# Kernel tuning notes

Hardware: AMD Instinct MI355X
Metric: run time of the kernel (lower is better)

Reference implementation:

```python
import jax, jax.numpy as jnp
import numpy as np
from jax.scipy.linalg import expm

S = 64          # alphabet size (codons)
M = 8           # number of models, prod(model_shape)
N_LEAVES = 32   # leaves of the balanced binary tree
N_EDGES = 62    # nodes 0..62, every non-root node has one parent edge (edge id == child node id)
B = 1024        # batch (alignment columns)
# per-level ranges of child-node ids; node 32+j has children (2j, 2j+1), etc.
LEVELS = [(0, 32), (32, 48), (48, 56), (56, 60), (60, 62)]


def inv_stereographic_projection(p):
    # maps R^{s-1} -> unit sphere S^{s-1}
    n2 = jnp.sum(p * p, axis=-1, keepdims=True)
    return jnp.concatenate([2.0 * p / (n2 + 1.0), (n2 - 1.0) / (n2 + 1.0)], axis=-1)


def generator(R, pi):
    # R: (M, s(s-1)/2) exchangeabilities, pi: (M, s) stationary distribution
    iu, ju = np.triu_indices(S, 1)
    A = jnp.zeros((M, S, S), R.dtype).at[:, iu, ju].set(R).at[:, ju, iu].set(R)
    Q = A * pi[:, None, :]                       # Q_ij = A_ij * pi_j (off-diagonal)
    row = jnp.sum(Q, axis=-1)                    # (M, S)
    return Q - jnp.eye(S, dtype=Q.dtype) * row[:, :, None]


def felsenstein(leave_configuration, R_inv, pi_inv, lengths):
    pi = inv_stereographic_projection(pi_inv) ** 2           # (M, S), rows sum to 1
    R = jnp.exp(R_inv)                                       # positive rates
    Q = generator(R, pi)                                     # (M, S, S)
    tQ = lengths[:, None, None, None] * Q[None]              # (E, M, S, S)
    P = jax.vmap(expm)(tQ.reshape(-1, S, S)).reshape(N_EDGES, M, S, S)
    # leaf alphas: tile leaf observations over the M models -> (n_leaves, B, M, S)
    prev = jnp.broadcast_to(
        leave_configuration.transpose(1, 0, 2)[:, :, None, :],
        (N_LEAVES, leave_configuration.shape[0], M, S))
    # level-synchronous pruning: messages up each parent edge, then product of the two children
    for a, b in LEVELS:
        msg = jnp.einsum('emcd,ebmd->ebmc', P[a:b], prev)    # per-edge transition
        prev = msg[0::2] * msg[1::2]                         # combine sibling pairs
    root = prev[0]                                           # (B, M, S)
    out = jnp.einsum('bms,ms->bm', root, pi)                 # P(data | model m)
    return out.reshape(out.shape[0], M)                      # (B, *model_shape)


def setup_inputs() -> dict:
    key = jax.random.key(0)
    k1, k2, k3, k4 = jax.random.split(key, 4)
    leave_configuration = jax.random.uniform(k1, (B, N_LEAVES, S), dtype=jnp.float32)
    tree_indices = jnp.zeros((B,), dtype=jnp.int32)          # single tree (F=1)
    R_inv = jax.random.uniform(k2, (M, S * (S - 1) // 2), dtype=jnp.float32,
                               minval=-1.0, maxval=1.0)
    pi_inv = jnp.full((M, S - 1), 1.0 / (np.sqrt(S) - 1.0), dtype=jnp.float32) \
        + 0.01 * jax.random.normal(k3, (M, S - 1), dtype=jnp.float32)
    lengths = jax.random.uniform(k4, (N_EDGES,), dtype=jnp.float32,
                                 minval=0.05, maxval=0.5)
    return {'leave_configuration': leave_configuration, 'R_inv': R_inv,
            'pi_inv': pi_inv, 'lengths': lengths, 'tree_indices': tree_indices}


def reference(leave_configuration, R_inv, pi_inv, lengths, tree_indices):
    # F=1: tf.dynamic_partition/gather_nd batch slicing is the identity, so
    # tree_indices is closed over / unused.
    return felsenstein(leave_configuration, R_inv, pi_inv, lengths)
```

## Files before the change

### kernel.cpp

```cpp
#include <hip/hip_runtime.h>

typedef unsigned short u16;
typedef unsigned int u32;
typedef __attribute__((ext_vector_type(8))) __bf16 bf16x8;
typedef __attribute__((ext_vector_type(4))) float f32x4;

constexpr size_t OFF_PI  = 0;
constexpr size_t OFF_PBH = 512;
constexpr size_t OFF_PBL = OFF_PBH + 1015808;

union FR { uint4 u; bf16x8 v; };

__device__ __forceinline__ void split_bf16(float x, u16& h, u16& l) {
  u32 b = __float_as_uint(x);
  u32 hb = (b + 0x7fffu + ((b >> 16) & 1u)) & 0xffff0000u;
  h = (u16)(hb >> 16);
  float r = x - __uint_as_float(hb);
  l = (u16)(__float_as_uint(r) >> 16);
}

__device__ __forceinline__ void split8(const f32x4 a, const f32x4 b,
                                       uint4& hi, uint4& lo) {
  u16 h[8], l[8];
  split_bf16(a.x, h[0], l[0]); split_bf16(a.y, h[1], l[1]);
  split_bf16(a.z, h[2], l[2]); split_bf16(a.w, h[3], l[3]);
  split_bf16(b.x, h[4], l[4]); split_bf16(b.y, h[5], l[5]);
  split_bf16(b.z, h[6], l[6]); split_bf16(b.w, h[7], l[7]);
  hi.x = h[0] | ((u32)h[1] << 16); hi.y = h[2] | ((u32)h[3] << 16);
  hi.z = h[4] | ((u32)h[5] << 16); hi.w = h[6] | ((u32)h[7] << 16);
  lo.x = l[0] | ((u32)l[1] << 16); lo.y = l[2] | ((u32)l[3] << 16);
  lo.z = l[4] | ((u32)l[5] << 16); lo.w = l[6] | ((u32)l[7] << 16);
}

__device__ __forceinline__ void mfma3(f32x4& a, const uint4 ah, const uint4 al,
                                      const uint4 bh, const uint4 bl) {
  FR Ah, Al, Bh, Bl;
  Ah.u = ah; Al.u = al; Bh.u = bh; Bl.u = bl;
  a = __builtin_amdgcn_mfma_f32_16x16x32_bf16(Ah.v, Bh.v, a, 0, 0, 0);
  a = __builtin_amdgcn_mfma_f32_16x16x32_bf16(Ah.v, Bl.v, a, 0, 0, 0);
  a = __builtin_amdgcn_mfma_f32_16x16x32_bf16(Al.v, Bh.v, a, 0, 0, 0);
}

__device__ __forceinline__ void xt_read2(const u32* b, int row, int chunk,
                                         uint4& hi, uint4& lo) {
  const int dw = (row << 5) + (((chunk + row) & 7) << 2);
  hi = *(const uint4*)&b[dw];
  lo = *(const uint4*)&b[2048 + dw];
}
__device__ __forceinline__ void xt_write4(u32* b, int row, int cp, int half,
                                          const f32x4 v) {
  u16 h[4], l[4];
  split_bf16(v.x, h[0], l[0]); split_bf16(v.y, h[1], l[1]);
  split_bf16(v.z, h[2], l[2]); split_bf16(v.w, h[3], l[3]);
  const int dw = (row << 5) + (((cp + row) & 7) << 2) + half * 2;
  uint2 hh, ll;
  hh.x = h[0] | ((u32)h[1] << 16); hh.y = h[2] | ((u32)h[3] << 16);
  ll.x = l[0] | ((u32)l[1] << 16); ll.y = l[2] | ((u32)l[3] << 16);
  *(uint2*)&b[dw] = hh;
  *(uint2*)&b[2048 + dw] = ll;
}

__global__ __launch_bounds__(1024) void k_pcomb(
    const float* __restrict__ R_inv, const float* __restrict__ pi_inv,
    const float* __restrict__ lengths, float* __restrict__ ws,
    u16* __restrict__ PBH, u16* __restrict__ PBL) {
  const int m = blockIdx.x & 7, prt = blockIdx.x >> 3;
  const int tid = threadIdx.x, lane = tid & 63, w = tid >> 6;
  const int ln = lane & 15, kq = lane >> 4;
  __shared__ float pis[64];
  __shared__ float n2s;
  __shared__ __align__(16) float Qs[64 * 68];
  __shared__ __align__(16) u32 PB[8][4096];

  if (tid < 64) {
    float p = (tid < 63) ? pi_inv[m * 63 + tid] : 0.f;
    float v = p * p;
    #pragma unroll
    for (int off = 32; off; off >>= 1) v += __shfl_down(v, off, 64);
    if (tid == 0) n2s = v;
  }
  __syncthreads();
  if (tid < 64) {
    const float den = n2s + 1.f;
    const float x = (tid < 63) ? 2.f * pi_inv[m * 63 + tid] / den
                               : (n2s - 1.f) / den;
    const float pv = x * x;
    pis[tid] = pv;
    if (prt == 0) ws[OFF_PI + (size_t)m * 64 + tid] = pv;
  }
  __syncthreads();
  for (int idx = tid; idx < 4096; idx += 1024) {
    const int i = idx >> 6, j = idx & 63;
    float q = 0.f;
    if (i != j) {
      const int a = min(i, j), b = max(i, j);
      const int kk = a * (127 - a) / 2 + (b - a - 1);
      q = expf(R_inv[m * 2016 + kk]) * pis[j];
    }
    Qs[i * 68 + j] = q;
  }
  __syncthreads();
  if (tid < 64) {
    float s = 0.f;
    #pragma unroll 4
    for (int j4 = 0; j4 < 64; j4 += 4) {
      const f32x4 q = *(const f32x4*)&Qs[tid * 68 + j4];
      s += q.x + q.y + q.z + q.w;
    }
    Qs[tid * 68 + tid] = -s;
  }
  __syncthreads();
  float q[12][4];
  const int ci0 = tid >> 4, cj0 = (tid & 15) * 4;
  #pragma unroll
  for (int r = 0; r < 4; ++r) q[0][r] = Qs[ci0 * 68 + cj0 + r];
  if (tid < 512) {
    const int i = tid >> 3, c = tid & 7;
    const f32x4 a = *(const f32x4*)&Qs[i * 68 + c * 8];
    const f32x4 b = *(const f32x4*)&Qs[i * 68 + c * 8 + 4];
    uint4 h, l;
    split8(a, b, h, l);
    const int dw = (i << 5) + (((c + i) & 7) << 2);
    *(uint4*)&PB[0][dw] = h;
    *(uint4*)&PB[0][2048 + dw] = l;
  } else {
    const int t2 = tid - 512, j = t2 >> 3, c = t2 & 7;
    f32x4 a, b;
    a.x = Qs[(c * 8 + 0) * 68 + j]; a.y = Qs[(c * 8 + 1) * 68 + j];
    a.z = Qs[(c * 8 + 2) * 68 + j]; a.w = Qs[(c * 8 + 3) * 68 + j];
    b.x = Qs[(c * 8 + 4) * 68 + j]; b.y = Qs[(c * 8 + 5) * 68 + j];
    b.z = Qs[(c * 8 + 6) * 68 + j]; b.w = Qs[(c * 8 + 7) * 68 + j];
    uint4 h, l;
    split8(a, b, h, l);
    const int dw = (j << 5) + (((c + j) & 7) << 2);
    *(uint4*)&PB[4][dw] = h;
    *(uint4*)&PB[4][2048 + dw] = l;
  }
  __syncthreads();

  const f32x4 z = {0.f, 0.f, 0.f, 0.f};
  const int ct = w >> 2, bt = w & 3;
  auto mm = [&](const u32* RX, const u32* CY, u32* dstC, u32* dstR) {
    uint4 ah[2], al[2], bh[2], bl[2];
    #pragma unroll
    for (int kh = 0; kh < 2; ++kh) {
      xt_read2(RX, ct * 16 + ln, kh * 4 + kq, ah[kh], al[kh]);
      xt_read2(CY, bt * 16 + ln, kh * 4 + kq, bh[kh], bl[kh]);
    }
    f32x4 a = z;
    #pragma unroll
    for (int kh = 0; kh < 2; ++kh) mfma3(a, ah[kh], al[kh], bh[kh], bl[kh]);
    #pragma unroll
    for (int r = 0; r < 4; ++r)
      Qs[(ct * 16 + kq * 4 + r) * 64 + bt * 16 + ln] = a[r];
    if (dstC) xt_write4(dstC, bt * 16 + ln, 2 * ct + (kq >> 1), kq & 1, a);
    if (dstR) {
      #pragma unroll
      for (int kh = 0; kh < 2; ++kh) {
        xt_read2(CY, ct * 16 + ln, kh * 4 + kq, ah[kh], al[kh]);
        xt_read2(RX, bt * 16 + ln, kh * 4 + kq, bh[kh], bl[kh]);
      }
      f32x4 a2 = z;
      #pragma unroll
      for (int kh = 0; kh < 2; ++kh) mfma3(a2, ah[kh], al[kh], bh[kh], bl[kh]);
      xt_write4(dstR, bt * 16 + ln, 2 * ct + (kq >> 1), kq & 1, a2);
    }
  };
  auto step = [&](const u32* RX, const u32* CY, int k, u32* dstC, u32* dstR) {
    mm(RX, CY, dstC, dstR);
    __syncthreads();
    #pragma unroll
    for (int r = 0; r < 4; ++r) q[k - 1][r] = Qs[tid * 4 + r];
    __syncthreads();
  };
  step(PB[0], PB[4], 2, PB[5], PB[1]);
  step(PB[1], PB[4], 3, PB[6], nullptr);
  step(PB[1], PB[5], 4, PB[7], PB[2]);
  step(PB[2], PB[4], 5, nullptr, nullptr);
  step(PB[2], PB[5], 6, nullptr, nullptr);
  step(PB[2], PB[6], 7, nullptr, nullptr);
  step(PB[2], PB[7], 8, nullptr, PB[3]);
  step(PB[3], PB[4], 9, nullptr, nullptr);
  step(PB[3], PB[5], 10, nullptr, nullptr);
  step(PB[3], PB[6], 11, nullptr, nullptr);
  step(PB[3], PB[7], 12, nullptr, nullptr);

  #pragma unroll
  for (int ei = 0; ei < 4; ++ei) {
    const int e = prt * 4 + ei;
    if (e >= 62) break;
    const float t = lengths[e];
    float av[4] = {0.f, 0.f, 0.f, 0.f};
    const int dr = ci0 - cj0;
    if (dr >= 0 && dr < 4) av[dr] = 1.f;
    float cf = 1.f;
    #pragma unroll
    for (int k = 1; k <= 12; ++k) {
      cf *= t / (float)k;
      #pragma unroll
      for (int r = 0; r < 4; ++r) av[r] = fmaf(cf, q[k - 1][r], av[r]);
    }
    u16 h[4], l[4];
    split_bf16(av[0], h[0], l[0]); split_bf16(av[1], h[1], l[1]);
    split_bf16(av[2], h[2], l[2]); split_bf16(av[3], h[3], l[3]);
    const size_t base = (((size_t)e * 8 + m) << 12) + tid * 4;
    ushort4 h4, l4;
    h4.x = h[0]; h4.y = h[1]; h4.z = h[2]; h4.w = h[3];
    l4.x = l[0]; l4.y = l[1]; l4.z = l[2]; l4.w = l[3];
    *(ushort4*)(PBH + base) = h4;
    *(ushort4*)(PBL + base) = l4;
  }
}

__global__ __launch_bounds__(512, 2) void k_tree(
    const float* __restrict__ leaves, const u16* __restrict__ Phi,
    const u16* __restrict__ Plo, const float* __restrict__ ws,
    float* __restrict__ out) {
  const int m = blockIdx.x & 7, btile = blockIdx.x >> 3;
  const int tid = threadIdx.x, lane = tid & 63, w = tid >> 6;
  const int ln = lane & 15, kq = lane >> 4;
  __shared__ __align__(16) u32 slots[16 * 2048];
  __shared__ float psum[2][4][16];
  const f32x4 z = {0.f, 0.f, 0.f, 0.f};

  auto node_read = [&](int slot, int row, int kh, uint4& bh, uint4& bl) {
    const int jc = kh * 8 + kq * 2;
    const u32* b = &slots[slot * 2048 + row * 64];
    const uint4 A = *(const uint4*)&b[((jc + row) & 15) << 2];
    const uint4 B = *(const uint4*)&b[((jc + 1 + row) & 15) << 2];
    bh.x = A.x; bh.y = A.y; bh.z = B.x; bh.w = B.y;
    bl.x = A.z; bl.y = A.w; bl.z = B.z; bl.w = B.w;
  };
  auto node_write = [&](int slot, int row, int jc, const f32x4 v) {
    u16 h[4], l[4];
    split_bf16(v.x, h[0], l[0]); split_bf16(v.y, h[1], l[1]);
    split_bf16(v.z, h[2], l[2]); split_bf16(v.w, h[3], l[3]);
    uint4 pk;
    pk.x = h[0] | ((u32)h[1] << 16); pk.y = h[2] | ((u32)h[3] << 16);
    pk.z = l[0] | ((u32)l[1] << 16); pk.w = l[2] | ((u32)l[3] << 16);
    *(uint4*)&slots[slot * 2048 + row * 64 + (((jc + row) & 15) << 2)] = pk;
  };

  auto do_pair = [&](int eb, int p, int s0, int s1, int outSlot, int bt0,
                     int nbt, int ct0, int nct, bool leaf, f32x4* rootout) {
    uint4 bfh[2][2][2], bfl[2][2][2];
    #pragma unroll
    for (int s = 0; s < 2; ++s)
      #pragma unroll
      for (int bi = 0; bi < 2; ++bi) {
        if (bi >= nbt) continue;
        const int row = (bt0 + bi) * 16 + ln;
        #pragma unroll
        for (int kh = 0; kh < 2; ++kh) {
          if (leaf) {
            const float* g = leaves + (size_t)(btile * 32 + row) * 2048 +
                             (size_t)(eb + 2 * p + s) * 64 + kh * 32 + kq * 8;
            const f32x4 xa = *(const f32x4*)g;
            const f32x4 xb = *(const f32x4*)(g + 4);
            split8(xa, xb, bfh[s][bi][kh], bfl[s][bi][kh]);
          } else {
            node_read(s ? s1 : s0, row, kh, bfh[s][bi][kh], bfl[s][bi][kh]);
          }
        }
      }
    uint4 ph[2][4][2], pl[2][4][2];
    #pragma unroll
    for (int s = 0; s < 2; ++s) {
      const size_t pb = ((size_t)(eb + 2 * p + s) * 8 + m) << 12;
      #pragma unroll
      for (int ci = 0; ci < 4; ++ci) {
        if (ci >= nct) continue;
        #pragma unroll
        for (int kh = 0; kh < 2; ++kh) {
          const size_t off =
              pb + (size_t)((ct0 + ci) * 16 + ln) * 64 + kh * 32 + kq * 8;
          ph[s][ci][kh] = *(const uint4*)(Phi + off);
          pl[s][ci][kh] = *(const uint4*)(Plo + off);
        }
      }
    }
    f32x4 a0[4][2];
    #pragma unroll
    for (int ci = 0; ci < 4; ++ci) {
      if (ci >= nct) continue;
      #pragma unroll
      for (int bi = 0; bi < 2; ++bi) {
        if (bi >= nbt) continue;
        f32x4 a = z;
        #pragma unroll
        for (int kh = 0; kh < 2; ++kh)
          mfma3(a, ph[0][ci][kh], pl[0][ci][kh], bfh[0][bi][kh], bfl[0][bi][kh]);
        a0[ci][bi] = a;
      }
    }
    #pragma unroll
    for (int ci = 0; ci < 4; ++ci) {
      if (ci >= nct) continue;
      #pragma unroll
      for (int bi = 0; bi < 2; ++bi) {
        if (bi >= nbt) continue;
        f32x4 a = z;
        #pragma unroll
        for (int kh = 0; kh < 2; ++kh)
          mfma3(a, ph[1][ci][kh], pl[1][ci][kh], bfh[1][bi][kh], bfl[1][bi][kh]);
        const f32x4 pr = a0[ci][bi] * a;
        if (rootout)
          *rootout = pr;
        else
          node_write(outSlot, (bt0 + bi) * 16 + ln, (ct0 + ci) * 4 + kq, pr);
      }
    }
  };

  do_pair(0, w, -1, -1, w, 0, 2, 0, 4, true, nullptr);
  do_pair(0, w + 8, -1, -1, w + 8, 0, 2, 0, 4, true, nullptr);
  __syncthreads();
  do_pair(32, w, 2 * w, 2 * w + 1, 2 * w, 0, 2, 0, 4, false, nullptr);
  __syncthreads();
  {
    const int j = w >> 1, bi = w & 1;
    do_pair(48, j, 4 * j, 4 * j + 2, 4 * j, bi, 1, 0, 4, false, nullptr);
  }
  __syncthreads();
  {
    const int j = w >> 2, bi = w & 1, ch = (w >> 1) & 1;
    do_pair(56, j, 8 * j, 8 * j + 4, 8 * j + 1, bi, 1, ch * 2, 2, false,
            nullptr);
  }
  __syncthreads();
  {
    f32x4 pr = z;
    do_pair(60, 0, 1, 9, -1, w & 1, 1, w >> 1, 1, false, &pr);
    const f32x4 piv =
        *(const f32x4*)&ws[OFF_PI + (size_t)m * 64 + (w >> 1) * 16 + kq * 4];
    float v = pr.x * piv.x + pr.y * piv.y + pr.z * piv.z + pr.w * piv.w;
    v += __shfl_xor(v, 16, 64);
    v += __shfl_xor(v, 32, 64);
    if (lane < 16) psum[w & 1][w >> 1][lane] = v;
  }
  __syncthreads();
  if (tid < 32) {
    const int bi = tid >> 4, bb = tid & 15;
    out[(size_t)(btile * 32 + tid) * 8 + m] =
        psum[bi][0][bb] + psum[bi][1][bb] + psum[bi][2][bb] + psum[bi][3][bb];
  }
}

extern "C" void kernel_launch(void* const* d_in, const int* in_sizes, int n_in,
                              void* d_out, int out_size, void* d_ws, size_t ws_size,
                              hipStream_t stream) {
  const float* leaves  = (const float*)d_in[0];
  const float* R_inv   = (const float*)d_in[1];
  const float* pi_inv  = (const float*)d_in[2];
  const float* lengths = (const float*)d_in[3];
  float* out = (float*)d_out;
  float* ws  = (float*)d_ws;

  u16* PBH = (u16*)(ws + OFF_PBH);
  u16* PBL = (u16*)(ws + OFF_PBL);

  hipLaunchKernelGGL(k_pcomb, dim3(128), dim3(1024), 0, stream, R_inv, pi_inv,
                     lengths, ws, PBH, PBL);
  hipLaunchKernelGGL(k_tree, dim3(256), dim3(512), 0, stream, leaves, PBH, PBL,
                     ws, out);
}
```

Before: 124.5 us.

## Reschedule tree kernel via depth-first table schedule with fewer LDS slots

The tree kernel now walks a precomputed schedule table that interleaves leaf pairs and internal merges depth-first. This lets it reuse 10 node slots instead of 16, and each wave now computes one 16x16 tile per pair. The smaller LDS footprint allows launch bounds of 4 blocks per CU instead of 2, which raises occupancy. The P-combination kernel drops one LDS buffer by reusing slot 0 and launches twice as many blocks, each handling 2 edges instead of 4, to spread the per-edge Taylor series work. In exchange the tree kernel has more barriers (11 phases instead of 5) and loops driven by a runtime table, with less unrolling.

After: 169.9 us. 36.5% more time.

```diff
diff --git a/kernel.cpp b/kernel.cpp
--- a/kernel.cpp
+++ b/kernel.cpp
@@ -70,7 +70,7 @@
   __shared__ float pis[64];
   __shared__ float n2s;
   __shared__ __align__(16) float Qs[64 * 68];
-  __shared__ __align__(16) u32 PB[8][4096];
+  __shared__ __align__(16) u32 PB[7][4096];
 
   if (tid < 64) {
     float p = (tid < 63) ? pi_inv[m * 63 + tid] : 0.f;
@@ -133,8 +133,8 @@
     uint4 h, l;
     split8(a, b, h, l);
     const int dw = (j << 5) + (((c + j) & 7) << 2);
-    *(uint4*)&PB[4][dw] = h;
-    *(uint4*)&PB[4][2048 + dw] = l;
+    *(uint4*)&PB[3][dw] = h;
+    *(uint4*)&PB[3][2048 + dw] = l;
   }
   __syncthreads();
 
@@ -173,21 +173,21 @@
     for (int r = 0; r < 4; ++r) q[k - 1][r] = Qs[tid * 4 + r];
     __syncthreads();
   };
-  step(PB[0], PB[4], 2, PB[5], PB[1]);
-  step(PB[1], PB[4], 3, PB[6], nullptr);
-  step(PB[1], PB[5], 4, PB[7], PB[2]);
-  step(PB[2], PB[4], 5, nullptr, nullptr);
-  step(PB[2], PB[5], 6, nullptr, nullptr);
-  step(PB[2], PB[6], 7, nullptr, nullptr);
-  step(PB[2], PB[7], 8, nullptr, PB[3]);
-  step(PB[3], PB[4], 9, nullptr, nullptr);
-  step(PB[3], PB[5], 10, nullptr, nullptr);
-  step(PB[3], PB[6], 11, nullptr, nullptr);
-  step(PB[3], PB[7], 12, nullptr, nullptr);
+  step(PB[0], PB[3], 2, PB[4], PB[1]);
+  step(PB[1], PB[3], 3, PB[5], nullptr);
+  step(PB[1], PB[4], 4, PB[6], PB[2]);
+  step(PB[2], PB[3], 5, nullptr, nullptr);
+  step(PB[2], PB[4], 6, nullptr, nullptr);
+  step(PB[2], PB[5], 7, nullptr, nullptr);
+  step(PB[2], PB[6], 8, nullptr, PB[0]);
+  step(PB[0], PB[3], 9, nullptr, nullptr);
+  step(PB[0], PB[4], 10, nullptr, nullptr);
+  step(PB[0], PB[5], 11, nullptr, nullptr);
+  step(PB[0], PB[6], 12, nullptr, nullptr);
 
   #pragma unroll
-  for (int ei = 0; ei < 4; ++ei) {
-    const int e = prt * 4 + ei;
+  for (int ei = 0; ei < 2; ++ei) {
+    const int e = prt * 2 + ei;
     if (e >= 62) break;
     const float t = lengths[e];
     float av[4] = {0.f, 0.f, 0.f, 0.f};
@@ -212,131 +212,108 @@
   }
 }
 
-__global__ __launch_bounds__(512, 2) void k_tree(
+#define SE(e, i0, i1, o) \
+  ((u32)(e) | ((u32)(i0) << 8) | ((u32)(i1) << 16) | ((u32)(o) << 24))
+__device__ const u32 SCHED[31] = {
+    SE(0, 0, 0, 0),   SE(2, 0, 0, 1),   SE(4, 0, 0, 2),   SE(6, 0, 0, 3),
+    SE(8, 0, 0, 4),   SE(10, 0, 0, 5),  SE(32, 0, 1, 6),  SE(34, 2, 3, 7),
+    SE(12, 0, 0, 8),  SE(14, 0, 0, 9),  SE(36, 4, 5, 0),  SE(48, 6, 7, 1),
+    SE(16, 0, 0, 2),  SE(18, 0, 0, 3),  SE(38, 8, 9, 4),  SE(20, 0, 0, 5),
+    SE(50, 0, 4, 6),  SE(40, 2, 3, 7),  SE(22, 0, 0, 8),  SE(24, 0, 0, 9),
+    SE(56, 1, 6, 0),  SE(42, 5, 8, 2),  SE(26, 0, 0, 3),  SE(28, 0, 0, 4),
+    SE(52, 7, 2, 1),  SE(44, 9, 3, 5),  SE(30, 0, 0, 6),  SE(46, 4, 6, 2),
+    SE(54, 5, 2, 3),  SE(58, 1, 3, 4),  SE(60, 0, 4, 15)};
+__device__ const int PH[12] = {0, 4, 8, 12, 16, 20, 24, 27, 28, 29, 30, 31};
+
+__global__ __launch_bounds__(512, 4) void k_tree(
     const float* __restrict__ leaves, const u16* __restrict__ Phi,
     const u16* __restrict__ Plo, const float* __restrict__ ws,
     float* __restrict__ out) {
   const int m = blockIdx.x & 7, btile = blockIdx.x >> 3;
   const int tid = threadIdx.x, lane = tid & 63, w = tid >> 6;
   const int ln = lane & 15, kq = lane >> 4;
-  __shared__ __align__(16) u32 slots[16 * 2048];
+  const int ct = w >> 1, bt = w & 1;
+  const int row = bt * 16 + ln;
+  __shared__ __align__(16) u32 slots[10 * 2048];
   __shared__ float psum[2][4][16];
   const f32x4 z = {0.f, 0.f, 0.f, 0.f};
-
-  auto node_read = [&](int slot, int row, int kh, uint4& bh, uint4& bl) {
-    const int jc = kh * 8 + kq * 2;
-    const u32* b = &slots[slot * 2048 + row * 64];
-    const uint4 A = *(const uint4*)&b[((jc + row) & 15) << 2];
-    const uint4 B = *(const uint4*)&b[((jc + 1 + row) & 15) << 2];
-    bh.x = A.x; bh.y = A.y; bh.z = B.x; bh.w = B.y;
-    bl.x = A.z; bl.y = A.w; bl.z = B.z; bl.w = B.w;
-  };
-  auto node_write = [&](int slot, int row, int jc, const f32x4 v) {
-    u16 h[4], l[4];
-    split_bf16(v.x, h[0], l[0]); split_bf16(v.y, h[1], l[1]);
-    split_bf16(v.z, h[2], l[2]); split_bf16(v.w, h[3], l[3]);
-    uint4 pk;
-    pk.x = h[0] | ((u32)h[1] << 16); pk.y = h[2] | ((u32)h[3] << 16);
-    pk.z = l[0] | ((u32)l[1] << 16); pk.w = l[2] | ((u32)l[3] << 16);
-    *(uint4*)&slots[slot * 2048 + row * 64 + (((jc + row) & 15) << 2)] = pk;
-  };
-
-  auto do_pair = [&](int eb, int p, int s0, int s1, int outSlot, int bt0,
-                     int nbt, int ct0, int nct, bool leaf, f32x4* rootout) {
-    uint4 bfh[2][2][2], bfl[2][2][2];
-    #pragma unroll
-    for (int s = 0; s < 2; ++s)
-      #pragma unroll
-      for (int bi = 0; bi < 2; ++bi) {
-        if (bi >= nbt) continue;
-        const int row = (bt0 + bi) * 16 + ln;
+  f32x4 rootpr = z;
+
+  for (int phx = 0; phx < 11; ++phx) {
+    const int pe = PH[phx + 1];
+    for (int idx = PH[phx]; idx < pe; ++idx) {
+      const u32 d = SCHED[idx];
+      const int e0 = d & 0xff, i0 = (d >> 8) & 0xff, i1 = (d >> 16) & 0xff,
+                os = d >> 24;
+      uint4 bh[2][2], bl[2][2];
+      if (e0 < 32) {
+        #pragma unroll
+        for (int s = 0; s < 2; ++s)
+          #pragma unroll
+          for (int kh = 0; kh < 2; ++kh) {
+            const float* g = leaves + (size_t)(btile * 32 + row) * 2048 +
+                             (size_t)(e0 + s) * 64 + kh * 32 + kq * 8;
+            const f32x4 xa = *(const f32x4*)g;
+            const f32x4 xb = *(const f32x4*)(g + 4);
+            split8(xa, xb, bh[s][kh], bl[s][kh]);
+          }
+      } else {
+        #pragma unroll
+        for (int s = 0; s < 2; ++s) {
+          const u32* nb = &slots[(s ? i1 : i0) * 2048 + row * 64];
+          #pragma unroll
+          for (int kh = 0; kh < 2; ++kh) {
+            const int jc = kh * 8 + kq * 2;
+            const uint4 A = *(const uint4*)&nb[((jc + row) & 15) << 2];
+            const uint4 B = *(const uint4*)&nb[((jc + 1 + row) & 15) << 2];
+            bh[s][kh].x = A.x; bh[s][kh].y = A.y;
+            bh[s][kh].z = B.x; bh[s][kh].w = B.y;
+            bl[s][kh].x = A.z; bl[s][kh].y = A.w;
+            bl[s][kh].z = B.z; bl[s][kh].w = B.w;
+          }
+        }
+      }
+      uint4 pfh[2][2], pfl[2][2];
+      #pragma unroll
+      for (int s = 0; s < 2; ++s) {
+        const size_t pb = ((size_t)(e0 + s) * 8 + m) << 12;
         #pragma unroll
         for (int kh = 0; kh < 2; ++kh) {
-          if (leaf) {
-            const float* g = leaves + (size_t)(btile * 32 + row) * 2048 +
-                             (size_t)(eb + 2 * p + s) * 64 + kh * 32 + kq * 8;
-            const f32x4 xa = *(const f32x4*)g;
-            const f32x4 xb = *(const f32x4*)(g + 4);
-            split8(xa, xb, bfh[s][bi][kh], bfl[s][bi][kh]);
-          } else {
-            node_read(s ? s1 : s0, row, kh, bfh[s][bi][kh], bfl[s][bi][kh]);
-          }
+          const size_t off = pb + (size_t)(ct * 16 + ln) * 64 + kh * 32 + kq * 8;
+          pfh[s][kh] = *(const uint4*)(Phi + off);
+          pfl[s][kh] = *(const uint4*)(Plo + off);
         }
       }
-    uint4 ph[2][4][2], pl[2][4][2];
-    #pragma unroll
-    for (int s = 0; s < 2; ++s) {
-      const size_t pb = ((size_t)(eb + 2 * p + s) * 8 + m) << 12;
-      #pragma unroll
-      for (int ci = 0; ci < 4; ++ci) {
-        if (ci >= nct) continue;
-        #pragma unroll
-        for (int kh = 0; kh < 2; ++kh) {
-          const size_t off =
-              pb + (size_t)((ct0 + ci) * 16 + ln) * 64 + kh * 32 + kq * 8;
-          ph[s][ci][kh] = *(const uint4*)(Phi + off);
-          pl[s][ci][kh] = *(const uint4*)(Plo + off);
-        }
-      }
-    }
-    f32x4 a0[4][2];
-    #pragma unroll
-    for (int ci = 0; ci < 4; ++ci) {
-      if (ci >= nct) continue;
-      #pragma unroll
-      for (int bi = 0; bi < 2; ++bi) {
-        if (bi >= nbt) continue;
-        f32x4 a = z;
-        #pragma unroll
-        for (int kh = 0; kh < 2; ++kh)
-          mfma3(a, ph[0][ci][kh], pl[0][ci][kh], bfh[0][bi][kh], bfl[0][bi][kh]);
-        a0[ci][bi] = a;
-      }
-    }
-    #pragma unroll
-    for (int ci = 0; ci < 4; ++ci) {
-      if (ci >= nct) continue;
-      #pragma unroll
-      for (int bi = 0; bi < 2; ++bi) {
-        if (bi >= nbt) continue;
-        f32x4 a = z;
-        #pragma unroll
-        for (int kh = 0; kh < 2; ++kh)
-          mfma3(a, ph[1][ci][kh], pl[1][ci][kh], bfh[1][bi][kh], bfl[1][bi][kh]);
-        const f32x4 pr = a0[ci][bi] * a;
-        if (rootout)
-          *rootout = pr;
-        else
-          node_write(outSlot, (bt0 + bi) * 16 + ln, (ct0 + ci) * 4 + kq, pr);
-      }
-    }
-  };
-
-  do_pair(0, w, -1, -1, w, 0, 2, 0, 4, true, nullptr);
-  do_pair(0, w + 8, -1, -1, w + 8, 0, 2, 0, 4, true, nullptr);
-  __syncthreads();
-  do_pair(32, w, 2 * w, 2 * w + 1, 2 * w, 0, 2, 0, 4, false, nullptr);
-  __syncthreads();
+      f32x4 a0 = z, a1 = z;
+      #pragma unroll
+      for (int kh = 0; kh < 2; ++kh) {
+        mfma3(a0, pfh[0][kh], pfl[0][kh], bh[0][kh], bl[0][kh]);
+        mfma3(a1, pfh[1][kh], pfl[1][kh], bh[1][kh], bl[1][kh]);
+      }
+      const f32x4 pr = a0 * a1;
+      if (os == 15) {
+        rootpr = pr;
+      } else {
+        u16 h[4], l[4];
+        split_bf16(pr.x, h[0], l[0]); split_bf16(pr.y, h[1], l[1]);
+        split_bf16(pr.z, h[2], l[2]); split_bf16(pr.w, h[3], l[3]);
+        uint4 pk;
+        pk.x = h[0] | ((u32)h[1] << 16); pk.y = h[2] | ((u32)h[3] << 16);
+        pk.z = l[0] | ((u32)l[1] << 16); pk.w = l[2] | ((u32)l[3] << 16);
+        const int jc = ct * 4 + kq;
+        *(uint4*)&slots[os * 2048 + row * 64 + (((jc + row) & 15) << 2)] = pk;
+      }
+    }
+    __syncthreads();
+  }
   {
-    const int j = w >> 1, bi = w & 1;
-    do_pair(48, j, 4 * j, 4 * j + 2, 4 * j, bi, 1, 0, 4, false, nullptr);
-  }
-  __syncthreads();
-  {
-    const int j = w >> 2, bi = w & 1, ch = (w >> 1) & 1;
-    do_pair(56, j, 8 * j, 8 * j + 4, 8 * j + 1, bi, 1, ch * 2, 2, false,
-            nullptr);
-  }
-  __syncthreads();
-  {
-    f32x4 pr = z;
-    do_pair(60, 0, 1, 9, -1, w & 1, 1, w >> 1, 1, false, &pr);
     const f32x4 piv =
-        *(const f32x4*)&ws[OFF_PI + (size_t)m * 64 + (w >> 1) * 16 + kq * 4];
-    float v = pr.x * piv.x + pr.y * piv.y + pr.z * piv.z + pr.w * piv.w;
+        *(const f32x4*)&ws[OFF_PI + (size_t)m * 64 + ct * 16 + kq * 4];
+    float v = rootpr.x * piv.x + rootpr.y * piv.y + rootpr.z * piv.z +
+              rootpr.w * piv.w;
     v += __shfl_xor(v, 16, 64);
     v += __shfl_xor(v, 32, 64);
-    if (lane < 16) psum[w & 1][w >> 1][lane] = v;
+    if (lane < 16) psum[bt][ct][lane] = v;
   }
   __syncthreads();
   if (tid < 32) {
@@ -359,7 +336,7 @@
   u16* PBH = (u16*)(ws + OFF_PBH);
   u16* PBL = (u16*)(ws + OFF_PBL);
 
-  hipLaunchKernelGGL(k_pcomb, dim3(128), dim3(1024), 0, stream, R_inv, pi_inv,
+  hipLaunchKernelGGL(k_pcomb, dim3(256), dim3(1024), 0, stream, R_inv, pi_inv,
                      lengths, ws, PBH, PBL);
   hipLaunchKernelGGL(k_tree, dim3(256), dim3(512), 0, stream, leaves, PBH, PBL,
                      ws, out);
```
